# Kernel tuning notes

Hardware: AMD Instinct MI355X
Metric: run time of the kernel (lower is better)

## Reference

```python
import jax, jax.numpy as jnp
import numpy as np

D_MODEL = 1024
D_STATE = 16
LN_EPS = 1e-5


def setup_inputs() -> dict:
    key = jax.random.key(0)
    ks = jax.random.split(key, 10)
    B, L, D, N = 4, 1024, D_MODEL, D_STATE
    s = lambda fan_in: 1.0 / np.sqrt(fan_in)
    x_in = jax.random.normal(ks[0], (B, L, D), dtype=jnp.float32)
    W_in = jax.random.uniform(ks[1], (D, 2 * D), jnp.float32, -s(D), s(D))
    W_x = jax.random.uniform(ks[2], (D, D + 2 * N), jnp.float32, -s(D), s(D))
    W_dt = jax.random.uniform(ks[3], (D, D), jnp.float32, -s(D), s(D))
    b_dt = jax.random.uniform(ks[4], (D,), jnp.float32, -4.0, -1.0)
    A_log = jnp.tile(jnp.log(jnp.arange(1, N + 1, dtype=jnp.float32))[None, :], (D, 1))
    D_param = jnp.ones((D,), dtype=jnp.float32)
    W_out = jax.random.uniform(ks[5], (D, D), jnp.float32, -s(D), s(D))
    ln_g = jnp.ones((D,), dtype=jnp.float32)
    ln_b = jnp.zeros((D,), dtype=jnp.float32)
    return {"x_in": x_in, "W_in": W_in, "W_x": W_x, "W_dt": W_dt, "b_dt": b_dt,
            "A_log": A_log, "D_param": D_param, "W_out": W_out, "ln_g": ln_g, "ln_b": ln_b}


def reference(x_in, W_in, W_x, W_dt, b_dt, A_log, D_param, W_out, ln_g, ln_b):
    B, L, D = x_in.shape
    N = A_log.shape[1]
    xz = x_in @ W_in                       # [B,L,2D]
    x, z = xz[..., :D], xz[..., D:]
    proj = x @ W_x                         # [B,L,D+2N]
    delta_raw = proj[..., :D]
    B_ssm = proj[..., D:D + N]
    C_ssm = proj[..., D + N:]
    delta = jax.nn.softplus(delta_raw @ W_dt + b_dt)   # [B,L,D]
    A = -jnp.exp(A_log)                    # [D,N]
    dA = jnp.exp(jnp.einsum('bld,dn->bldn', delta, A))      # [B,L,D,N]
    dBx = jnp.einsum('bld,bln->bldn', delta * x, B_ssm)      # dB * x, fused

    def step(h, inp):
        dA_t, dBx_t, C_t = inp             # [B,D,N],[B,D,N],[B,N]
        h = dA_t * h + dBx_t
        y_t = jnp.einsum('bdn,bn->bd', h, C_t)
        return h, y_t

    h0 = jnp.zeros((B, D, N), dtype=x.dtype)
    xs = (jnp.moveaxis(dA, 1, 0), jnp.moveaxis(dBx, 1, 0), jnp.moveaxis(C_ssm, 1, 0))
    _, ys = jax.lax.scan(step, h0, xs)     # ys: [L,B,D]
    y = jnp.moveaxis(ys, 0, 1) + x * D_param
    y = (y * jax.nn.silu(z)) @ W_out
    res = y + x_in
    mu = jnp.mean(res, axis=-1, keepdims=True)
    var = jnp.var(res, axis=-1, keepdims=True)
    return (res - mu) * jax.lax.rsqrt(var + LN_EPS) * ln_g + ln_b
```

## Files before the change

### kernel.cpp

```cpp
#include <hip/hip_runtime.h>

#define D_MODEL 1024
#define D_STATE 16
#define M_ROWS  4096
#define SEQ_L   1024
#define NSEG    64
#define LSEG    16

typedef __bf16 bf16x8 __attribute__((ext_vector_type(8)));
typedef float  f32x4  __attribute__((ext_vector_type(4)));

__device__ __forceinline__ unsigned short f2bf(float f) {
  unsigned int u = __builtin_bit_cast(unsigned int, f);
  u += 0x7fffu + ((u >> 16) & 1u);
  return (unsigned short)(u >> 16);
}
__device__ __forceinline__ float bf2f(unsigned short b) {
  unsigned int u = ((unsigned int)b) << 16;
  return __builtin_bit_cast(float, u);
}
__device__ __forceinline__ float load_elem(const void* p, size_t i, int isbf) {
  if (isbf) return bf2f(((const unsigned short*)p)[i]);
  return ((const float*)p)[i];
}

__device__ __forceinline__ int is_bf16(const void* x_in) {
  unsigned int v = ((const unsigned short*)x_in)[2 * (threadIdx.x & 63)];
  unsigned int e = (v >> 7) & 0xFFu;
  unsigned long long m = __ballot(e >= 100u && e <= 135u);
  return __popcll(m) >= 32;
}

__device__ __forceinline__ void gload16(const void* g, void* l) {
  typedef const __attribute__((address_space(1))) unsigned int GU;
  typedef __attribute__((address_space(3))) unsigned int LU;
  __builtin_amdgcn_global_load_lds((GU*)(unsigned long long)g,
                                   (LU*)(unsigned int)(unsigned long long)l,
                                   16, 0, 0);
}

__global__ void prep_kernel(const void* __restrict__ x_in, unsigned short* __restrict__ x_b,
                            const void* __restrict__ W_in, const void* __restrict__ W_x,
                            const void* __restrict__ W_dt, const void* __restrict__ W_out,
                            unsigned short* __restrict__ wx_raw,
                            unsigned short* __restrict__ wt_in, unsigned short* __restrict__ wt_xbc,
                            unsigned short* __restrict__ wt_dt, unsigned short* __restrict__ wt_out,
                            const void* b_dt, const void* A_log, const void* Dp,
                            const void* ln_g, const void* ln_b,
                            float* o_bdt, float* o_a2, float* o_dp,
                            float* o_lng, float* o_lnb) {
  __shared__ float tile[32][33];
  const int isbf = is_bf16(x_in);
  const int bid = blockIdx.x;
  const int tid = threadIdx.x;
  if (bid < 2048 || (bid >= 2128 && bid < 2656)) {
    const void* src; unsigned short* dst; int c;
    if (bid < 2048) { src = x_in; dst = x_b; c = bid * 256 + tid; }
    else { src = W_x; dst = wx_raw; c = (bid - 2128) * 256 + tid; }
    if (isbf) {
      ((uint4*)dst)[c] = ((const uint4*)src)[c];
    } else {
      float4 a = ((const float4*)src)[2 * c];
      float4 b = ((const float4*)src)[2 * c + 1];
      uint4 p;
      p.x = (unsigned int)f2bf(a.x) | ((unsigned int)f2bf(a.y) << 16);
      p.y = (unsigned int)f2bf(a.z) | ((unsigned int)f2bf(a.w) << 16);
      p.z = (unsigned int)f2bf(b.x) | ((unsigned int)f2bf(b.y) << 16);
      p.w = (unsigned int)f2bf(b.z) | ((unsigned int)f2bf(b.w) << 16);
      ((uint4*)dst)[c] = p;
    }
  } else if (bid < 2128) {
    int g = (bid - 2048) * 256 + tid;
    if (g < 1024)              o_bdt[g]          = load_elem(b_dt, g, isbf);
    else if (g < 17408) {
      float v = load_elem(A_log, g - 1024, isbf);
      o_a2[g - 1024] = -expf(v) * 1.4426950408889634f;
    }
    else if (g < 18432)        o_dp[g - 17408]   = load_elem(Dp, g - 17408, isbf);
    else if (g < 19456)        o_lng[g - 18432]  = load_elem(ln_g, g - 18432, isbf);
    else                       o_lnb[g - 19456]  = load_elem(ln_b, g - 19456, isbf);
  } else {
    int t = bid - 2656;
    const void* src; unsigned short* dst; int ncols, col0, bxx, byy;
    if (t < 2048)      { src = W_in;  dst = wt_in;  ncols = 2048; col0 = 0;
                         bxx = t & 63; byy = t >> 6; }
    else if (t < 2176) { t -= 2048; src = W_x; dst = wt_xbc; ncols = 1056; col0 = 1024;
                         bxx = t & 3; byy = t >> 2; }
    else if (t < 3200) { t -= 2176; src = W_dt; dst = wt_dt; ncols = 1024; col0 = 0;
                         bxx = t & 31; byy = t >> 5; }
    else               { t -= 3200; src = W_out; dst = wt_out; ncols = 1024; col0 = 0;
                         bxx = t & 31; byy = t >> 5; }
    int tx = tid & 31, ty = tid >> 5;
    int n0 = col0 + bxx * 32, k0 = byy * 32;
    #pragma unroll
    for (int r = 0; r < 4; ++r) {
      int k = k0 + ty + r * 8;
      int n = n0 + tx;
      float v = (n < ncols) ? load_elem(src, (size_t)k * ncols + n, isbf) : 0.f;
      tile[ty + r * 8][tx] = v;
    }
    __syncthreads();
    #pragma unroll
    for (int r = 0; r < 4; ++r) {
      int n = n0 + ty + r * 8;
      int k = k0 + tx;
      dst[(size_t)(n - col0) * 1024 + k] = f2bf(tile[tx][ty + r * 8]);
    }
  }
}

template<int MODE>
__global__ __launch_bounds__(256, 3) void gemm_bf(
    const unsigned short* __restrict__ A, const unsigned short* __restrict__ Bt, int ldb,
    void* __restrict__ o0, void* __restrict__ o1, void* __restrict__ o2,
    float* __restrict__ o3, float* __restrict__ o4,
    const float* __restrict__ aux, const void* __restrict__ auxv,
    const unsigned short* __restrict__ A_u, const unsigned short* __restrict__ B_u,
    int ldb_u, void* __restrict__ o_u) {
  __shared__ __align__(16) unsigned short a_lds[3][128 * 32];
  __shared__ __align__(16) unsigned short b_lds[3][128 * 32];
  const int isbf = (MODE == 4) ? is_bf16(auxv) : 0;
  const int tid = threadIdx.x;
  const int wave = tid >> 6, lane = tid & 63;
  const int wr = (wave >> 1) * 64, wc = (wave & 1) * 64;
  const int lrow = lane & 15, quad = lane >> 4;

  int m0, n0, ldbl = ldb;
  const unsigned short* Asrc = A;
  const unsigned short* Bsrc = Bt;
  bool isU = false;
  if (MODE == 1 && blockIdx.x >= 32) {
    isU = true;
    int u = (blockIdx.x - 32) * 16 + blockIdx.y;
    m0 = (u >> 3) * 128; n0 = (u & 7) * 128;
    Asrc = A_u; Bsrc = B_u; ldbl = ldb_u;
  } else {
    m0 = blockIdx.x * 128; n0 = blockIdx.y * 128;
    if (MODE == 2 && n0 >= 1024) { Bsrc = (const unsigned short*)o2; n0 -= 1024; }
  }
  const int nout = (MODE == 2 && Bsrc == (const unsigned short*)o2) ? n0 + 1024 : n0;

  const int sc = (lane & 3) ^ ((lane >> 3) & 3);
  const unsigned short* gA  = Asrc + (size_t)(m0 + wave * 32 + (lane >> 2)) * 1024 + sc * 8;
  const unsigned short* gA2 = gA + (size_t)16 * 1024;
  const unsigned short* gB  = Bsrc + (size_t)(n0 + wave * 32 + (lane >> 2)) * ldbl + sc * 8;
  const unsigned short* gB2 = gB + (size_t)16 * ldbl;
  const int q2 = quad ^ ((lrow >> 1) & 3);

  f32x4 acc[4][4];
  #pragma unroll
  for (int i = 0; i < 4; ++i)
    #pragma unroll
    for (int j = 0; j < 4; ++j)
      #pragma unroll
      for (int r = 0; r < 4; ++r) acc[i][j][r] = 0.f;

  auto issue = [&](int k) {
    unsigned short* ab = a_lds[k % 3] + wave * 32 * 32;
    unsigned short* bb = b_lds[k % 3] + wave * 32 * 32;
    gload16(gA + k * 32, ab);
    gload16(gA2 + k * 32, ab + 16 * 32);
    gload16(gB + k * 32, bb);
    gload16(gB2 + k * 32, bb + 16 * 32);
  };
  auto compute = [&](int k) {
    const unsigned short* ard = a_lds[k % 3] + (wr + lrow) * 32 + q2 * 8;
    const unsigned short* brd = b_lds[k % 3] + (wc + lrow) * 32 + q2 * 8;
    bf16x8 af[4], bfr[4];
    #pragma unroll
    for (int i = 0; i < 4; ++i) af[i] = *(const bf16x8*)(ard + i * 16 * 32);
    #pragma unroll
    for (int j = 0; j < 4; ++j) bfr[j] = *(const bf16x8*)(brd + j * 16 * 32);
    #pragma unroll
    for (int i = 0; i < 4; ++i)
      #pragma unroll
      for (int j = 0; j < 4; ++j)
        acc[i][j] = __builtin_amdgcn_mfma_f32_16x16x32_bf16(af[i], bfr[j], acc[i][j], 0, 0, 0);
  };

  issue(0);
  issue(1);
  #pragma unroll
  for (int k = 0; k < 31; ++k) {
    asm volatile("s_waitcnt vmcnt(4)" ::: "memory");
    __builtin_amdgcn_s_barrier();
    if (k + 2 < 32) issue(k + 2);
    compute(k);
  }
  asm volatile("s_waitcnt vmcnt(0)" ::: "memory");
  __builtin_amdgcn_s_barrier();
  compute(31);

  #pragma unroll
  for (int i = 0; i < 4; ++i) {
    #pragma unroll
    for (int jj = 0; jj < 4; ++jj) {
      #pragma unroll
      for (int r = 0; r < 4; ++r) {
        int m = m0 + wr + i * 16 + quad * 4 + r;
        int n = nout + wc + jj * 16 + lrow;
        float v = acc[i][jj][r];
        if (MODE == 1) {
          if (isU) {
            ((unsigned short*)o_u)[(size_t)m * 1024 + n] = f2bf(v);
          } else if (n < 1024) {
            ((unsigned short*)o0)[(size_t)m * 1024 + n] = f2bf(v);
          } else {
            float sig = 1.f / (1.f + expf(-v));
            ((unsigned short*)o1)[(size_t)m * 1024 + (n - 1024)] = f2bf(v * sig);
          }
        } else if (MODE == 2) {
          if (n < 1024) {
            float t = v + aux[n];
            float sp = (t > 20.f) ? t : log1pf(expf(t));
            ((unsigned short*)o0)[(size_t)m * 1024 + n] = f2bf(sp);
          }
          else if (n < 1040)  o3[(size_t)m * D_STATE + (n - 1024)] = v;
          else if (n < 1056)  o4[(size_t)m * D_STATE + (n - 1040)] = v;
        } else {
          ((float*)o0)[(size_t)m * 1024 + n] =
              v + load_elem(auxv, (size_t)m * 1024 + n, isbf);
        }
      }
    }
  }
}

template<int PHASE>
__global__ __launch_bounds__(256) void scan_phase(
    const unsigned short* __restrict__ dl_bf, const unsigned short* __restrict__ x_bf,
    const unsigned short* __restrict__ z_bf, const float* __restrict__ Bs,
    const float* __restrict__ Cs, const float* __restrict__ A2g,
    const float* __restrict__ Dpar, const float* __restrict__ hinit,
    float* __restrict__ Hout, float* __restrict__ sdout,
    unsigned short* __restrict__ g) {
  __shared__ float4 bsh[LSEG][4];
  __shared__ float4 csh[LSEG][4];
  const int tid = threadIdx.x;
  const int bid = blockIdx.x;
  const int seg = bid >> 4;
  const int b = (bid >> 2) & 3;
  const int dc = bid & 3;
  const int d = dc * 256 + tid;
  const int t0 = seg * LSEG;
  const int bd = b * D_MODEL + d;

  if (tid < LSEG * 4) {
    int r = tid >> 2, q = tid & 3;
    size_t src = ((size_t)b * SEQ_L + t0 + r) * 4 + q;
    bsh[r][q] = ((const float4*)Bs)[src];
    if (PHASE == 1) csh[r][q] = ((const float4*)Cs)[src];
  }

  float A2r[16];
  {
    const float4* a4 = (const float4*)(A2g + (size_t)d * 16);
    #pragma unroll
    for (int q = 0; q < 4; ++q) {
      float4 v = a4[q];
      A2r[4*q] = v.x; A2r[4*q+1] = v.y; A2r[4*q+2] = v.z; A2r[4*q+3] = v.w;
    }
  }
  float h[16];
  if (PHASE == 1) {
    const float4* h4 = (const float4*)(hinit + (((size_t)seg * 4096) + bd) * 16);
    #pragma unroll
    for (int q = 0; q < 4; ++q) {
      float4 v = h4[q];
      h[4*q] = v.x; h[4*q+1] = v.y; h[4*q+2] = v.z; h[4*q+3] = v.w;
    }
  } else {
    #pragma unroll
    for (int n = 0; n < 16; ++n) h[n] = 0.f;
  }
  const float Dpd = (PHASE == 1) ? Dpar[d] : 0.f;
  float sd = 0.f;
  const size_t base = ((size_t)b * SEQ_L + t0) * D_MODEL + d;
  __syncthreads();

  unsigned short dreg[2][8], xreg[2][8], zreg[2][8];
  #pragma unroll
  for (int t = 0; t < 8; ++t) {
    size_t o = base + (size_t)t * D_MODEL;
    dreg[0][t] = dl_bf[o]; xreg[0][t] = x_bf[o];
    if (PHASE == 1) zreg[0][t] = z_bf[o];
  }
  #pragma unroll
  for (int c = 0; c < LSEG / 8; ++c) {
    const int cur = c & 1, nxt = cur ^ 1;
    if (c < LSEG / 8 - 1) {
      #pragma unroll
      for (int t = 0; t < 8; ++t) {
        size_t o = base + (size_t)((c + 1) * 8 + t) * D_MODEL;
        dreg[nxt][t] = dl_bf[o]; xreg[nxt][t] = x_bf[o];
        if (PHASE == 1) zreg[nxt][t] = z_bf[o];
      }
    }
    #pragma unroll
    for (int t = 0; t < 8; ++t) {
      const int tt = c * 8 + t;
      float dl = bf2f(dreg[cur][t]);
      float xx = bf2f(xreg[cur][t]);
      float dx = dl * xx;
      sd += dl;
      float4 b0 = bsh[tt][0], b1 = bsh[tt][1], b2 = bsh[tt][2], b3 = bsh[tt][3];
      float bb[16] = {b0.x,b0.y,b0.z,b0.w, b1.x,b1.y,b1.z,b1.w,
                      b2.x,b2.y,b2.z,b2.w, b3.x,b3.y,b3.z,b3.w};
      if (PHASE == 0) {
        #pragma unroll
        for (int n = 0; n < 16; ++n) {
          float dA = exp2f(dl * A2r[n]);
          h[n] = fmaf(dA, h[n], dx * bb[n]);
        }
      } else {
        float4 c0 = csh[tt][0], c1 = csh[tt][1], c2 = csh[tt][2], c3 = csh[tt][3];
        float cc[16] = {c0.x,c0.y,c0.z,c0.w, c1.x,c1.y,c1.z,c1.w,
                        c2.x,c2.y,c2.z,c2.w, c3.x,c3.y,c3.z,c3.w};
        float y = 0.f;
        #pragma unroll
        for (int n = 0; n < 16; ++n) {
          float dA = exp2f(dl * A2r[n]);
          h[n] = fmaf(dA, h[n], dx * bb[n]);
          y = fmaf(h[n], cc[n], y);
        }
        float zz = bf2f(zreg[cur][t]);
        g[base + (size_t)tt * D_MODEL] = f2bf(fmaf(xx, Dpd, y) * zz);
      }
    }
  }
  if (PHASE == 0) {
    float4* ho = (float4*)(Hout + (((size_t)seg * 4096) + bd) * 16);
    #pragma unroll
    for (int q = 0; q < 4; ++q)
      ho[q] = make_float4(h[4*q], h[4*q+1], h[4*q+2], h[4*q+3]);
    sdout[(size_t)seg * 4096 + bd] = sd;
  }
}

__global__ __launch_bounds__(256) void scan_phaseB(
    const float* __restrict__ H, const float* __restrict__ sdelta,
    const float* __restrict__ A2g, float* __restrict__ hinit) {
  int gidx = blockIdx.x * 256 + threadIdx.x;
  int bd = gidx >> 4, n = gidx & 15;
  float A2 = A2g[(size_t)(bd & (D_MODEL - 1)) * 16 + n];
  float hp = 0.f;
  #pragma unroll 8
  for (int s = 0; s < NSEG; ++s) {
    size_t idx = ((size_t)s * 4096 + bd) * 16 + n;
    hinit[idx] = hp;
    float P = exp2f(A2 * sdelta[(size_t)s * 4096 + bd]);
    hp = fmaf(P, hp, H[idx]);
  }
}

__global__ __launch_bounds__(256) void ln_kernel(const float* __restrict__ res,
    const float* __restrict__ lng, const float* __restrict__ lnb,
    void* __restrict__ out, const void* __restrict__ x_in) {
  const int isbf = is_bf16(x_in);
  int row = blockIdx.x, tid = threadIdx.x;
  const float4* r4 = (const float4*)(res + (size_t)row * D_MODEL);
  float4 v = r4[tid];
  float s = v.x + v.y + v.z + v.w;
  float q = v.x * v.x + v.y * v.y + v.z * v.z + v.w * v.w;
  #pragma unroll
  for (int m = 1; m < 64; m <<= 1) { s += __shfl_xor(s, m); q += __shfl_xor(q, m); }
  __shared__ float ss[4], qs[4];
  int w = tid >> 6;
  if ((tid & 63) == 0) { ss[w] = s; qs[w] = q; }
  __syncthreads();
  s = ss[0] + ss[1] + ss[2] + ss[3];
  q = qs[0] + qs[1] + qs[2] + qs[3];
  float mu = s * (1.f / D_MODEL);
  float var = q * (1.f / D_MODEL) - mu * mu;
  float rstd = rsqrtf(var + 1e-5f);
  float4 gg = ((const float4*)lng)[tid];
  float4 bb = ((const float4*)lnb)[tid];
  float o0 = (v.x - mu) * rstd * gg.x + bb.x;
  float o1 = (v.y - mu) * rstd * gg.y + bb.y;
  float o2 = (v.z - mu) * rstd * gg.z + bb.z;
  float o3 = (v.w - mu) * rstd * gg.w + bb.w;
  if (isbf) {
    ushort4 pv;
    pv.x = f2bf(o0); pv.y = f2bf(o1); pv.z = f2bf(o2); pv.w = f2bf(o3);
    ((ushort4*)out)[(size_t)row * 256 + tid] = pv;
  } else {
    ((float4*)out)[(size_t)row * 256 + tid] = make_float4(o0, o1, o2, o3);
  }
}

extern "C" void kernel_launch(void* const* d_in, const int* in_sizes, int n_in,
                              void* d_out, int out_size, void* d_ws, size_t ws_size,
                              hipStream_t stream) {
  (void)in_sizes; (void)n_in; (void)out_size; (void)ws_size;
  const void* x_in  = d_in[0];
  const void* W_in  = d_in[1];
  const void* W_x   = d_in[2];
  const void* W_dt  = d_in[3];
  const void* b_dt  = d_in[4];
  const void* A_log = d_in[5];
  const void* D_par = d_in[6];
  const void* W_out = d_in[7];
  const void* ln_g  = d_in[8];
  const void* ln_b  = d_in[9];

  char* ws = (char*)d_ws;
  size_t off = 0;
  auto alloc = [&](size_t bytes) -> void* {
    void* p = ws + off;
    off += (bytes + 255) & ~(size_t)255;
    return p;
  };
  unsigned short* x_in_b  = (unsigned short*)alloc((size_t)M_ROWS * D_MODEL * 2);
  unsigned short* wx_raw  = (unsigned short*)alloc((size_t)1024 * 1056 * 2);
  float* bdt_f            = (float*)alloc(1024 * 4);
  float* a2_f             = (float*)alloc(16384 * 4);
  float* dp_f             = (float*)alloc(1024 * 4);
  float* lng_f            = (float*)alloc(1024 * 4);
  float* lnb_f            = (float*)alloc(1024 * 4);
  unsigned short* wt_in   = (unsigned short*)alloc((size_t)2048 * 1024 * 2);
  unsigned short* wt_xbc  = (unsigned short*)alloc((size_t)128 * 1024 * 2);
  unsigned short* wt_dt   = (unsigned short*)alloc((size_t)1024 * 1024 * 2);
  unsigned short* wt_out  = (unsigned short*)alloc((size_t)1024 * 1024 * 2);
  unsigned short* U_bf    = (unsigned short*)alloc((size_t)1024 * 1024 * 2);
  unsigned short* x_bf    = (unsigned short*)alloc((size_t)M_ROWS * D_MODEL * 2);
  unsigned short* s_bf    = (unsigned short*)alloc((size_t)M_ROWS * D_MODEL * 2);
  unsigned short* delta_bf= (unsigned short*)alloc((size_t)M_ROWS * D_MODEL * 2);
  unsigned short* g_bf    = (unsigned short*)alloc((size_t)M_ROWS * D_MODEL * 2);
  float* bssm_f           = (float*)alloc((size_t)M_ROWS * D_STATE * 4);
  float* cssm_f           = (float*)alloc((size_t)M_ROWS * D_STATE * 4);
  float* H_f              = (float*)alloc((size_t)NSEG * 4096 * 16 * 4);
  float* hinit_f          = (float*)alloc((size_t)NSEG * 4096 * 16 * 4);
  float* sdelta_f         = (float*)alloc((size_t)NSEG * 4096 * 4);
  float* res_f = (float*)x_bf;

  prep_kernel<<<6880, 256, 0, stream>>>(x_in, x_in_b, W_in, W_x, W_dt, W_out,
                                        wx_raw, wt_in, wt_xbc, wt_dt, wt_out,
                                        b_dt, A_log, D_par, ln_g, ln_b,
                                        bdt_f, a2_f, dp_f, lng_f, lnb_f);

  gemm_bf<1><<<dim3(36, 16), 256, 0, stream>>>(x_in_b, wt_in, 1024,
      x_bf, s_bf, nullptr, nullptr, nullptr, nullptr, nullptr,
      wt_dt, wx_raw, 1056, U_bf);

  gemm_bf<2><<<dim3(32, 9), 256, 0, stream>>>(x_bf, U_bf, 1024,
      delta_bf, nullptr, wt_xbc, bssm_f, cssm_f, bdt_f, nullptr,
      nullptr, nullptr, 0, nullptr);

  scan_phase<0><<<1024, 256, 0, stream>>>(delta_bf, x_bf, nullptr, bssm_f, nullptr,
                                          a2_f, nullptr, nullptr, H_f, sdelta_f, nullptr);
  scan_phaseB<<<256, 256, 0, stream>>>(H_f, sdelta_f, a2_f, hinit_f);
  scan_phase<1><<<1024, 256, 0, stream>>>(delta_bf, x_bf, s_bf, bssm_f, cssm_f,
                                          a2_f, dp_f, hinit_f, nullptr, nullptr, g_bf);

  gemm_bf<4><<<dim3(32, 8), 256, 0, stream>>>(g_bf, wt_out, 1024,
      res_f, nullptr, nullptr, nullptr, nullptr, nullptr, x_in,
      nullptr, nullptr, 0, nullptr);

  ln_kernel<<<4096, 256, 0, stream>>>(res_f, lng_f, lnb_f, d_out, x_in);
}
```

Before: 270.7 us.

## Use 64-row tiles for later GEMMs and 4-stage pipeline for input GEMM

For the delta and output GEMMs, the M tile is halved to 64 rows, which doubles the grid (64x9 and 64x8 blocks) and raises the launch-bounds occupancy hint to 4. The input-projection GEMM keeps 128-row tiles but moves to a 4-buffer LDS ring with three tiles prefetched, with vmcnt waits adjusted to match. The smaller tiles aim to fill more of the GPU's compute units on grids that are otherwise small. In exchange they lower arithmetic intensity per block, and the deeper pipeline uses more LDS, which can limit occupancy.

```diff
diff --git a/kernel.cpp b/kernel.cpp
--- a/kernel.cpp
+++ b/kernel.cpp
@@ -110,19 +110,23 @@
 }
 
 template<int MODE>
-__global__ __launch_bounds__(256, 3) void gemm_bf(
+__global__ __launch_bounds__(256, MODE == 1 ? 2 : 4) void gemm_bf(
     const unsigned short* __restrict__ A, const unsigned short* __restrict__ Bt, int ldb,
     void* __restrict__ o0, void* __restrict__ o1, void* __restrict__ o2,
     float* __restrict__ o3, float* __restrict__ o4,
     const float* __restrict__ aux, const void* __restrict__ auxv,
     const unsigned short* __restrict__ A_u, const unsigned short* __restrict__ B_u,
     int ldb_u, void* __restrict__ o_u) {
-  __shared__ __align__(16) unsigned short a_lds[3][128 * 32];
-  __shared__ __align__(16) unsigned short b_lds[3][128 * 32];
+  constexpr int BM   = (MODE == 1) ? 128 : 64;
+  constexpr int NBUF = (MODE == 1) ? 4 : 3;
+  constexpr int AW   = (MODE == 1) ? 32 : 16;
+  constexpr int MI   = (MODE == 1) ? 4 : 2;
+  __shared__ __align__(16) unsigned short a_lds[NBUF][BM * 32];
+  __shared__ __align__(16) unsigned short b_lds[NBUF][128 * 32];
   const int isbf = (MODE == 4) ? is_bf16(auxv) : 0;
   const int tid = threadIdx.x;
   const int wave = tid >> 6, lane = tid & 63;
-  const int wr = (wave >> 1) * 64, wc = (wave & 1) * 64;
+  const int wr = (wave >> 1) * (MI * 16), wc = (wave & 1) * 64;
   const int lrow = lane & 15, quad = lane >> 4;
 
   int m0, n0, ldbl = ldb;
@@ -135,64 +139,75 @@
     m0 = (u >> 3) * 128; n0 = (u & 7) * 128;
     Asrc = A_u; Bsrc = B_u; ldbl = ldb_u;
   } else {
-    m0 = blockIdx.x * 128; n0 = blockIdx.y * 128;
+    m0 = blockIdx.x * BM; n0 = blockIdx.y * 128;
     if (MODE == 2 && n0 >= 1024) { Bsrc = (const unsigned short*)o2; n0 -= 1024; }
   }
   const int nout = (MODE == 2 && Bsrc == (const unsigned short*)o2) ? n0 + 1024 : n0;
 
   const int sc = (lane & 3) ^ ((lane >> 3) & 3);
-  const unsigned short* gA  = Asrc + (size_t)(m0 + wave * 32 + (lane >> 2)) * 1024 + sc * 8;
+  const unsigned short* gA  = Asrc + (size_t)(m0 + wave * AW + (lane >> 2)) * 1024 + sc * 8;
   const unsigned short* gA2 = gA + (size_t)16 * 1024;
   const unsigned short* gB  = Bsrc + (size_t)(n0 + wave * 32 + (lane >> 2)) * ldbl + sc * 8;
   const unsigned short* gB2 = gB + (size_t)16 * ldbl;
   const int q2 = quad ^ ((lrow >> 1) & 3);
 
-  f32x4 acc[4][4];
+  f32x4 acc[MI][4];
   #pragma unroll
-  for (int i = 0; i < 4; ++i)
+  for (int i = 0; i < MI; ++i)
     #pragma unroll
     for (int j = 0; j < 4; ++j)
       #pragma unroll
       for (int r = 0; r < 4; ++r) acc[i][j][r] = 0.f;
 
   auto issue = [&](int k) {
-    unsigned short* ab = a_lds[k % 3] + wave * 32 * 32;
-    unsigned short* bb = b_lds[k % 3] + wave * 32 * 32;
+    unsigned short* ab = a_lds[k % NBUF] + wave * AW * 32;
+    unsigned short* bb = b_lds[k % NBUF] + wave * 32 * 32;
     gload16(gA + k * 32, ab);
-    gload16(gA2 + k * 32, ab + 16 * 32);
+    if (MODE == 1) gload16(gA2 + k * 32, ab + 16 * 32);
     gload16(gB + k * 32, bb);
     gload16(gB2 + k * 32, bb + 16 * 32);
   };
   auto compute = [&](int k) {
-    const unsigned short* ard = a_lds[k % 3] + (wr + lrow) * 32 + q2 * 8;
-    const unsigned short* brd = b_lds[k % 3] + (wc + lrow) * 32 + q2 * 8;
-    bf16x8 af[4], bfr[4];
-    #pragma unroll
-    for (int i = 0; i < 4; ++i) af[i] = *(const bf16x8*)(ard + i * 16 * 32);
+    const unsigned short* ard = a_lds[k % NBUF] + (wr + lrow) * 32 + q2 * 8;
+    const unsigned short* brd = b_lds[k % NBUF] + (wc + lrow) * 32 + q2 * 8;
+    bf16x8 af[MI], bfr[4];
+    #pragma unroll
+    for (int i = 0; i < MI; ++i) af[i] = *(const bf16x8*)(ard + i * 16 * 32);
     #pragma unroll
     for (int j = 0; j < 4; ++j) bfr[j] = *(const bf16x8*)(brd + j * 16 * 32);
     #pragma unroll
-    for (int i = 0; i < 4; ++i)
+    for (int i = 0; i < MI; ++i)
       #pragma unroll
       for (int j = 0; j < 4; ++j)
         acc[i][j] = __builtin_amdgcn_mfma_f32_16x16x32_bf16(af[i], bfr[j], acc[i][j], 0, 0, 0);
   };
 
-  issue(0);
-  issue(1);
-  #pragma unroll
-  for (int k = 0; k < 31; ++k) {
-    asm volatile("s_waitcnt vmcnt(4)" ::: "memory");
-    __builtin_amdgcn_s_barrier();
-    if (k + 2 < 32) issue(k + 2);
-    compute(k);
+  if constexpr (MODE == 1) {
+    issue(0); issue(1); issue(2);
+    #pragma unroll
+    for (int k = 0; k < 31; ++k) {
+      if (k < 30) asm volatile("s_waitcnt vmcnt(8)" ::: "memory");
+      else        asm volatile("s_waitcnt vmcnt(4)" ::: "memory");
+      __builtin_amdgcn_s_barrier();
+      if (k + 3 < 32) issue(k + 3);
+      compute(k);
+    }
+  } else {
+    issue(0); issue(1);
+    #pragma unroll
+    for (int k = 0; k < 31; ++k) {
+      asm volatile("s_waitcnt vmcnt(3)" ::: "memory");
+      __builtin_amdgcn_s_barrier();
+      if (k + 2 < 32) issue(k + 2);
+      compute(k);
+    }
   }
   asm volatile("s_waitcnt vmcnt(0)" ::: "memory");
   __builtin_amdgcn_s_barrier();
   compute(31);
 
   #pragma unroll
-  for (int i = 0; i < 4; ++i) {
+  for (int i = 0; i < MI; ++i) {
     #pragma unroll
     for (int jj = 0; jj < 4; ++jj) {
       #pragma unroll
@@ -442,7 +457,7 @@
       x_bf, s_bf, nullptr, nullptr, nullptr, nullptr, nullptr,
       wt_dt, wx_raw, 1056, U_bf);
 
-  gemm_bf<2><<<dim3(32, 9), 256, 0, stream>>>(x_bf, U_bf, 1024,
+  gemm_bf<2><<<dim3(64, 9), 256, 0, stream>>>(x_bf, U_bf, 1024,
       delta_bf, nullptr, wt_xbc, bssm_f, cssm_f, bdt_f, nullptr,
       nullptr, nullptr, 0, nullptr);
 
@@ -452,7 +467,7 @@
   scan_phase<1><<<1024, 256, 0, stream>>>(delta_bf, x_bf, s_bf, bssm_f, cssm_f,
                                           a2_f, dp_f, hinit_f, nullptr, nullptr, g_bf);
 
-  gemm_bf<4><<<dim3(32, 8), 256, 0, stream>>>(g_bf, wt_out, 1024,
+  gemm_bf<4><<<dim3(64, 8), 256, 0, stream>>>(g_bf, wt_out, 1024,
       res_f, nullptr, nullptr, nullptr, nullptr, nullptr, x_in,
       nullptr, nullptr, 0, nullptr);
 
```

Measured after the change: 262.0 us. 3.2% less time.
